# Kernel optimization log

Measured on AMD Instinct MI355X. Metric: run time of the kernel, lower is better.

The kernel has to match this reference:

```python
import jax, jax.numpy as jnp
import numpy as np

B, T, C = 4, 2048, 1024
NH = 16
HD = C // NH  # 64

def setup_inputs() -> dict:
    key = jax.random.key(0)
    k1, k2, k3 = jax.random.split(key, 3)
    x = jax.random.normal(k1, (B, T, C), dtype=jnp.float32)
    w_qkv = jax.random.normal(k2, (C, 3 * C), dtype=jnp.float32) * (1.0 / np.sqrt(C))
    w_out = jax.random.normal(k3, (C, C), dtype=jnp.float32) * (1.0 / np.sqrt(C))
    b_out = jnp.zeros((C,), dtype=jnp.float32)
    return {"x": x, "w_qkv": w_qkv, "w_out": w_out, "b_out": b_out}

def reference(x, w_qkv, w_out, b_out):
    b, t, c = x.shape
    nh, hd = NH, c // NH
    qkv = x @ w_qkv                      # [b, t, 3c]
    q, k, v = jnp.split(qkv, 3, axis=-1)
    # [b, t, c] -> [b, nh, t, hd]
    def heads(z):
        return z.reshape(b, t, nh, hd).transpose(0, 2, 1, 3)
    q, k, v = heads(q), heads(k), heads(v)
    scale = 1.0 / jnp.sqrt(jnp.asarray(hd, dtype=x.dtype))
    scores = jnp.einsum('bhqd,bhkd->bhqk', q, k) * scale  # [b, nh, t, t]
    causal = jnp.tril(jnp.ones((t, t), dtype=bool))
    scores = jnp.where(causal, scores, jnp.asarray(-jnp.inf, dtype=scores.dtype))
    attn = jax.nn.softmax(scores, axis=-1)
    ctx = jnp.einsum('bhqk,bhkd->bhqd', attn, v)           # [b, nh, t, hd]
    ctx = ctx.transpose(0, 2, 1, 3).reshape(b, t, c)
    return ctx @ w_out + b_out
```

## Files before the change

kernel.cpp:

```cpp
#include <hip/hip_runtime.h>
#include <cmath>


typedef __bf16 bf16x4 __attribute__((ext_vector_type(4)));
typedef __bf16 bf16x8 __attribute__((ext_vector_type(8)));
typedef float  f32x4  __attribute__((ext_vector_type(4)));
typedef float  f32x16 __attribute__((ext_vector_type(16)));

__device__ __forceinline__ void gload_lds16(const __bf16* g, __bf16* l) {
    __builtin_amdgcn_global_load_lds(
        (const __attribute__((address_space(1))) void*)g,
        (__attribute__((address_space(3))) void*)l,
        16, 0, 0);
}

__global__ __launch_bounds__(256) void cast_bf16(const float* __restrict__ in,
                                                 __bf16* __restrict__ out, int n4) {
    int i = blockIdx.x * 256 + threadIdx.x;
    if (i >= n4) return;
    float4 f = *(const float4*)(in + (size_t)i * 4);
    bf16x4 o;
    o[0] = (__bf16)f.x; o[1] = (__bf16)f.y; o[2] = (__bf16)f.z; o[3] = (__bf16)f.w;
    *(bf16x4*)(out + (size_t)i * 4) = o;
}

__global__ __launch_bounds__(256) void transpose_cast(const float* __restrict__ W,
                                                      __bf16* __restrict__ WT,
                                                      int K, int N) {
    __shared__ float tile[32][33];
    const int n0 = blockIdx.x * 32, k0 = blockIdx.y * 32;
    const int tx = threadIdx.x & 31, ty = threadIdx.x >> 5;
    #pragma unroll
    for (int i = 0; i < 4; ++i)
        tile[ty + 8 * i][tx] = W[(size_t)(k0 + ty + 8 * i) * N + n0 + tx];
    __syncthreads();
    #pragma unroll
    for (int i = 0; i < 4; ++i)
        WT[(size_t)(n0 + ty + 8 * i) * K + k0 + tx] = (__bf16)tile[tx][ty + 8 * i];
}

__global__ __launch_bounds__(256) void transpose_v(const __bf16* __restrict__ qkv,
                                                   __bf16* __restrict__ Vt) {
    constexpr int T = 2048, R3C = 3072;
    __shared__ __bf16 tile[64][72];
    const int bh = blockIdx.y;
    const int b  = bh >> 4, h = bh & 15;
    const int kt = blockIdx.x * 64;
    const int tid = threadIdx.x;
    #pragma unroll
    for (int i = 0; i < 2; ++i) {
        int idx = tid + 256 * i;
        int kr  = idx >> 3;
        int c8  = idx & 7;
        *(uint4*)&tile[kr][c8 * 8] =
            *(const uint4*)(qkv + (size_t)(b * T + kt + kr) * R3C + 2048 + h * 64 + c8 * 8);
    }
    __syncthreads();
    #pragma unroll
    for (int i = 0; i < 2; ++i) {
        int idx = tid + 256 * i;
        int d   = idx >> 3;
        int k8  = idx & 7;
        union { __bf16 v[8]; uint4 u; } t;
        #pragma unroll
        for (int j = 0; j < 8; ++j) t.v[j] = tile[k8 * 8 + j][d];
        *(uint4*)(Vt + ((size_t)bh * 64 + d) * T + kt + k8 * 8) = t.u;
    }
}

template <typename OutT, bool BIAS>
__global__ __launch_bounds__(256) void gemm_bt(const __bf16* __restrict__ A,
                                               const __bf16* __restrict__ BT,
                                               OutT* __restrict__ Cc,
                                               const float* __restrict__ bias,
                                               int M, int N, int K) {
    __shared__ __bf16 As[128 * 32];
    __shared__ __bf16 Bs[128 * 32];

    const int tid  = threadIdx.x;
    const int lane = tid & 63;
    const int w    = tid >> 6;
    const int wr   = w >> 1, wc = w & 1;
    const int cc   = lane & 15, gg = lane >> 4;
    const int rowBase = blockIdx.y * 128;
    const int colBase = blockIdx.x * 128;

    f32x4 acc[4][4];
    #pragma unroll
    for (int i = 0; i < 4; ++i)
        #pragma unroll
        for (int j = 0; j < 4; ++j) acc[i][j] = f32x4{0.f, 0.f, 0.f, 0.f};

    for (int k0 = 0; k0 < K; k0 += 32) {
        __syncthreads();
        #pragma unroll
        for (int i = 0; i < 2; ++i) {
            int idx = tid + 256 * i;
            int r   = idx >> 2;
            int c4  = idx & 3;
            gload_lds16(A  + (size_t)(rowBase + r) * K + k0 + c4 * 8, &As[idx * 8]);
            gload_lds16(BT + (size_t)(colBase + r) * K + k0 + c4 * 8, &Bs[idx * 8]);
        }
        __syncthreads();

        bf16x8 af[4], bfr[4];
        #pragma unroll
        for (int i = 0; i < 4; ++i)
            af[i] = *(const bf16x8*)&As[(wr * 64 + i * 16 + cc) * 32 + gg * 8];
        #pragma unroll
        for (int j = 0; j < 4; ++j)
            bfr[j] = *(const bf16x8*)&Bs[(wc * 64 + j * 16 + cc) * 32 + gg * 8];
        #pragma unroll
        for (int i = 0; i < 4; ++i)
            #pragma unroll
            for (int j = 0; j < 4; ++j)
                acc[i][j] = __builtin_amdgcn_mfma_f32_16x16x32_bf16(af[i], bfr[j], acc[i][j], 0, 0, 0);
    }

    #pragma unroll
    for (int i = 0; i < 4; ++i)
        #pragma unroll
        for (int j = 0; j < 4; ++j) {
            const int col = colBase + wc * 64 + j * 16 + cc;
            #pragma unroll
            for (int r = 0; r < 4; ++r) {
                const int row = rowBase + wr * 64 + i * 16 + gg * 4 + r;
                float v = acc[i][j][r];
                if (BIAS) v += bias[col];
                Cc[(size_t)row * N + col] = (OutT)v;
            }
        }
}

__global__ __launch_bounds__(256) void flash_attn_mfma(const __bf16* __restrict__ qkv,
                                                       const __bf16* __restrict__ Vt,
                                                       __bf16* __restrict__ ctx) {
    constexpr int T = 2048, C = 1024, NH = 16, HD = 64;
    constexpr int R3C = 3 * C;
    constexpr float K1 = 0.125f * 1.44269504088896f;
    constexpr float K2 = -16.0f * 1.44269504088896f;

    const int tid  = threadIdx.x;
    const int lane = tid & 63;
    const int w    = tid >> 6;
    const int q5   = lane & 31;
    const int half = lane >> 5;

    const int bh   = blockIdx.x;
    const int y    = blockIdx.y;
    const int qtA  = 15 - y;
    const int qtB  = y;
    const int b    = bh >> 4;
    const int h    = bh & 15;
    const int srowA = qtA * 128 + w * 32;
    const int srowB = qtB * 128 + w * 32;
    const int ktmaxA = qtA * 128 + 64;
    const int ktmaxB = qtB * 128 + 64;

    __shared__ __attribute__((aligned(16))) __bf16 Ks [64][72];
    __shared__ __attribute__((aligned(16))) __bf16 VsT[64][72];
    __shared__ __attribute__((aligned(16))) __bf16 Ps [4][32][72];

    const __bf16* QrowA = qkv + (size_t)(b * T + srowA + q5) * R3C + h * HD;
    const __bf16* QrowB = qkv + (size_t)(b * T + srowB + q5) * R3C + h * HD;
    bf16x8 QbA[4], QbB[4];
    #pragma unroll
    for (int ks = 0; ks < 4; ++ks) {
        QbA[ks] = *(const bf16x8*)(QrowA + ks * 16 + half * 8);
        QbB[ks] = *(const bf16x8*)(QrowB + ks * 16 + half * 8);
    }

    f32x16 OA[2], OB[2];
    #pragma unroll
    for (int mb = 0; mb < 2; ++mb)
        #pragma unroll
        for (int r = 0; r < 16; ++r) { OA[mb][r] = 0.f; OB[mb][r] = 0.f; }
    float lsumA = 0.f, lsumB = 0.f;

    const __bf16* Kb  = qkv + (size_t)(b * T) * R3C + C + h * HD;
    const __bf16* Vtb = Vt + (size_t)bh * 64 * T;

    for (int kt = 0; kt <= ktmaxA; kt += 64) {
        __syncthreads();
        #pragma unroll
        for (int i = 0; i < 2; ++i) {
            int idx = tid + 256 * i;
            int kr  = idx >> 3;
            int c8  = idx & 7;
            *(uint4*)&Ks[kr][c8 * 8] = *(const uint4*)(Kb + (size_t)(kt + kr) * R3C + c8 * 8);
        }
        #pragma unroll
        for (int i = 0; i < 2; ++i) {
            int idx = tid + 256 * i;
            int d   = idx >> 3;
            int k8  = idx & 7;
            *(uint4*)&VsT[d][k8 * 8] = *(const uint4*)(Vtb + (size_t)d * T + kt + k8 * 8);
        }
        __syncthreads();

        #pragma unroll
        for (int sub = 0; sub < 2; ++sub) {
            f32x16 S;
            #pragma unroll
            for (int r = 0; r < 16; ++r) S[r] = 0.f;
            #pragma unroll
            for (int ks = 0; ks < 4; ++ks) {
                bf16x8 kb = *(const bf16x8*)&Ks[sub * 32 + q5][ks * 16 + half * 8];
                S = __builtin_amdgcn_mfma_f32_32x32x16_bf16(kb, QbA[ks], S, 0, 0, 0);
            }
            if (kt + sub * 32 + 31 > srowA) {
                #pragma unroll
                for (int r = 0; r < 16; ++r) {
                    int key = kt + sub * 32 + (r & 3) + 8 * (r >> 2) + 4 * half;
                    if (key > srowA + q5) S[r] = -1e30f;
                }
            }
            #pragma unroll
            for (int a = 0; a < 4; ++a) {
                union { bf16x4 v; uint2 u; } pk;
                #pragma unroll
                for (int bq = 0; bq < 4; ++bq) {
                    float p = exp2f(fmaf(S[4 * a + bq], K1, K2));
                    lsumA += p;
                    pk.v[bq] = (__bf16)p;
                }
                *(uint2*)&Ps[w][q5][sub * 32 + 8 * a + 4 * half] = pk.u;
            }
        }
        #pragma unroll
        for (int ks2 = 0; ks2 < 4; ++ks2) {
            bf16x8 pa = *(const bf16x8*)&Ps[w][q5][ks2 * 16 + half * 8];
            #pragma unroll
            for (int mb = 0; mb < 2; ++mb) {
                bf16x8 vb = *(const bf16x8*)&VsT[mb * 32 + q5][ks2 * 16 + half * 8];
                OA[mb] = __builtin_amdgcn_mfma_f32_32x32x16_bf16(vb, pa, OA[mb], 0, 0, 0);
            }
        }

        if (kt <= ktmaxB) {
            #pragma unroll
            for (int sub = 0; sub < 2; ++sub) {
                f32x16 S;
                #pragma unroll
                for (int r = 0; r < 16; ++r) S[r] = 0.f;
                #pragma unroll
                for (int ks = 0; ks < 4; ++ks) {
                    bf16x8 kb = *(const bf16x8*)&Ks[sub * 32 + q5][ks * 16 + half * 8];
                    S = __builtin_amdgcn_mfma_f32_32x32x16_bf16(kb, QbB[ks], S, 0, 0, 0);
                }
                if (kt + sub * 32 + 31 > srowB) {
                    #pragma unroll
                    for (int r = 0; r < 16; ++r) {
                        int key = kt + sub * 32 + (r & 3) + 8 * (r >> 2) + 4 * half;
                        if (key > srowB + q5) S[r] = -1e30f;
                    }
                }
                #pragma unroll
                for (int a = 0; a < 4; ++a) {
                    union { bf16x4 v; uint2 u; } pk;
                    #pragma unroll
                    for (int bq = 0; bq < 4; ++bq) {
                        float p = exp2f(fmaf(S[4 * a + bq], K1, K2));
                        lsumB += p;
                        pk.v[bq] = (__bf16)p;
                    }
                    *(uint2*)&Ps[w][q5][sub * 32 + 8 * a + 4 * half] = pk.u;
                }
            }
            #pragma unroll
            for (int ks2 = 0; ks2 < 4; ++ks2) {
                bf16x8 pa = *(const bf16x8*)&Ps[w][q5][ks2 * 16 + half * 8];
                #pragma unroll
                for (int mb = 0; mb < 2; ++mb) {
                    bf16x8 vb = *(const bf16x8*)&VsT[mb * 32 + q5][ks2 * 16 + half * 8];
                    OB[mb] = __builtin_amdgcn_mfma_f32_32x32x16_bf16(vb, pa, OB[mb], 0, 0, 0);
                }
            }
        }
    }

    const float invA = 1.f / (lsumA + __shfl_xor(lsumA, 32));
    const float invB = 1.f / (lsumB + __shfl_xor(lsumB, 32));

    __bf16* crowA = ctx + (size_t)(b * T + srowA + q5) * C + h * HD;
    __bf16* crowB = ctx + (size_t)(b * T + srowB + q5) * C + h * HD;
    #pragma unroll
    for (int mb = 0; mb < 2; ++mb)
        #pragma unroll
        for (int a = 0; a < 4; ++a) {
            union { bf16x4 v; uint2 u; } pA, pB;
            #pragma unroll
            for (int bq = 0; bq < 4; ++bq) {
                pA.v[bq] = (__bf16)(OA[mb][4 * a + bq] * invA);
                pB.v[bq] = (__bf16)(OB[mb][4 * a + bq] * invB);
            }
            *(uint2*)(crowA + mb * 32 + 8 * a + 4 * half) = pA.u;
            *(uint2*)(crowB + mb * 32 + 8 * a + 4 * half) = pB.u;
        }
}

extern "C" void kernel_launch(void* const* d_in, const int* in_sizes, int n_in,
                              void* d_out, int out_size, void* d_ws, size_t ws_size,
                              hipStream_t stream) {
    constexpr int B = 4, T = 2048, C = 1024;
    constexpr int M = B * T;

    const float* x     = (const float*)d_in[0];
    const float* w_qkv = (const float*)d_in[1];
    const float* w_out = (const float*)d_in[2];
    const float* b_out = (const float*)d_in[3];
    float* out = (float*)d_out;

    char* ws = (char*)d_ws;
    __bf16* xb     = (__bf16*)(ws);
    __bf16* wqkvT  = (__bf16*)(ws + (16ull << 20));
    __bf16* woutT  = (__bf16*)(ws + (22ull << 20));
    __bf16* qkvb   = (__bf16*)(ws + (24ull << 20));
    __bf16* ctxb   = (__bf16*)(ws + (72ull << 20));
    __bf16* Vt     = (__bf16*)(ws + (88ull << 20));

    cast_bf16<<<(M * C / 4 + 255) / 256, 256, 0, stream>>>(x, xb, M * C / 4);
    transpose_cast<<<dim3(3 * C / 32, C / 32), 256, 0, stream>>>(w_qkv, wqkvT, C, 3 * C);
    transpose_cast<<<dim3(C / 32, C / 32), 256, 0, stream>>>(w_out, woutT, C, C);

    gemm_bt<__bf16, false><<<dim3(3 * C / 128, M / 128), 256, 0, stream>>>(
        xb, wqkvT, qkvb, nullptr, M, 3 * C, C);

    transpose_v<<<dim3(T / 64, B * 16), 256, 0, stream>>>(qkvb, Vt);

    flash_attn_mfma<<<dim3(B * 16, 8), 256, 0, stream>>>(qkvb, Vt, ctxb);

    gemm_bt<float, true><<<dim3(C / 128, M / 128), 256, 0, stream>>>(
        ctxb, woutT, out, b_out, M, C, C);
}
```

Baseline: 286.5 us.

## Add pipelined 256x256 QKV GEMM and keep attention P in registers

```diff
diff --git a/kernel.cpp b/kernel.cpp
--- a/kernel.cpp
+++ b/kernel.cpp
@@ -13,6 +13,20 @@
         (__attribute__((address_space(3))) void*)l,
         16, 0, 0);
 }
+
+__device__ __forceinline__ unsigned packbf(float a, float b) {
+    union { __bf16 h[2]; unsigned u; } t;
+    t.h[0] = (__bf16)a; t.h[1] = (__bf16)b;
+    return t.u;
+}
+
+__device__ __forceinline__ void permswap(unsigned& a, unsigned& b) {
+    asm volatile("v_permlane32_swap_b32 %0, %1" : "+v"(a), "+v"(b));
+}
+
+#define BAR()  __builtin_amdgcn_s_barrier()
+#define VM2()  { asm volatile("s_waitcnt vmcnt(2)" ::: "memory"); \
+                 __builtin_amdgcn_sched_barrier(0); }
 
 __global__ __launch_bounds__(256) void cast_bf16(const float* __restrict__ in,
                                                  __bf16* __restrict__ out, int n4) {
@@ -68,6 +82,121 @@
     }
 }
 
+__global__ __launch_bounds__(512) void gemm256(const __bf16* __restrict__ A,
+                                               const __bf16* __restrict__ BT,
+                                               __bf16* __restrict__ Cc,
+                                               int M, int N, int K) {
+    __shared__ __attribute__((aligned(16))) char lds[131072];
+    const int tid = threadIdx.x, lane = tid & 63, w = tid >> 6;
+    const int wr = w >> 2, wc = w & 3, cc = lane & 15, gg = lane >> 4;
+
+    const int cpx = gridDim.x >> 3;
+    const int swz = ((int)blockIdx.x & 7) * cpx + ((int)blockIdx.x >> 3);
+    const int nbx = N >> 8;
+    const int rowBase = (swz / nbx) << 8;
+    const int colBase = (swz % nbx) << 8;
+    const int NT = K >> 6;
+
+    const int sChunk = (lane & 7) ^ (lane >> 3);
+    const int rsub   = lane >> 3;
+
+    auto stA = [&](int t, int h) {
+        const int buf = t & 1, k0 = (t % NT) * 64;
+        #pragma unroll
+        for (int l = 0; l < 2; ++l) {
+            int idx   = l * 8 + w;
+            int rbase = ((idx >> 3) << 7) + h * 64 + ((idx & 7) << 3);
+            gload_lds16(A + (size_t)(rowBase + rbase + rsub) * K + k0 + sChunk * 8,
+                        (__bf16*)(lds + buf * 65536 + rbase * 128 + lane * 16));
+        }
+    };
+    auto stB = [&](int t, int h) {
+        const int buf = t & 1, k0 = (t % NT) * 64;
+        #pragma unroll
+        for (int l = 0; l < 2; ++l) {
+            int idx   = l * 8 + w;
+            int rbase = ((idx >> 2) << 6) + h * 32 + ((idx & 3) << 3);
+            gload_lds16(BT + (size_t)(colBase + rbase + rsub) * K + k0 + sChunk * 8,
+                        (__bf16*)(lds + buf * 65536 + 32768 + rbase * 128 + lane * 16));
+        }
+    };
+
+    f32x4 acc[8][4];
+    #pragma unroll
+    for (int i = 0; i < 8; ++i)
+        #pragma unroll
+        for (int j = 0; j < 4; ++j) acc[i][j] = f32x4{0.f, 0.f, 0.f, 0.f};
+    bf16x8 afr[8], bfr[8];
+
+    auto rdA = [&](int buf, int mh) {
+        const char* base = lds + buf * 65536;
+        #pragma unroll
+        for (int i = 0; i < 4; ++i)
+            #pragma unroll
+            for (int kk = 0; kk < 2; ++kk) {
+                int r  = wr * 128 + mh * 64 + i * 16 + cc;
+                int cb = (kk * 64 + gg * 16) ^ ((cc & 7) << 4);
+                afr[i * 2 + kk] = *(const bf16x8*)(base + r * 128 + cb);
+            }
+    };
+    auto rdB = [&](int buf) {
+        const char* base = lds + buf * 65536 + 32768;
+        #pragma unroll
+        for (int j = 0; j < 4; ++j)
+            #pragma unroll
+            for (int kk = 0; kk < 2; ++kk) {
+                int r  = wc * 64 + j * 16 + cc;
+                int cb = (kk * 64 + gg * 16) ^ ((cc & 7) << 4);
+                bfr[j * 2 + kk] = *(const bf16x8*)(base + r * 128 + cb);
+            }
+    };
+
+#define QMFMA(MH, NH)                                                        \
+    _Pragma("unroll") for (int i = 0; i < 4; ++i)                            \
+    _Pragma("unroll") for (int j = 0; j < 2; ++j)                            \
+    _Pragma("unroll") for (int kk = 0; kk < 2; ++kk)                         \
+        acc[(MH)*4 + i][(NH)*2 + j] = __builtin_amdgcn_mfma_f32_16x16x32_bf16( \
+            afr[i*2 + kk], bfr[((NH)*2 + j)*2 + kk], acc[(MH)*4 + i][(NH)*2 + j], 0, 0, 0);
+
+    stA(0, 0); stB(0, 0); stA(0, 1); stB(0, 1); stA(1, 0);
+    VM2(); BAR();
+
+    for (int t = 0; t < NT; ++t) {
+        const int buf = t & 1;
+        rdA(buf, 0); rdB(buf);
+        stB(t + 1, 0);
+        BAR();
+        __builtin_amdgcn_s_setprio(1); QMFMA(0, 0); __builtin_amdgcn_s_setprio(0);
+        BAR();
+        stA(t + 1, 1);
+        BAR();
+        __builtin_amdgcn_s_setprio(1); QMFMA(0, 1); __builtin_amdgcn_s_setprio(0);
+        BAR();
+        rdA(buf, 1);
+        stB(t + 1, 1);
+        BAR();
+        __builtin_amdgcn_s_setprio(1); QMFMA(1, 0); __builtin_amdgcn_s_setprio(0);
+        BAR();
+        stA(t + 2, 0);
+        BAR();
+        __builtin_amdgcn_s_setprio(1); QMFMA(1, 1); __builtin_amdgcn_s_setprio(0);
+        VM2(); BAR();
+    }
+#undef QMFMA
+
+    #pragma unroll
+    for (int i = 0; i < 8; ++i)
+        #pragma unroll
+        for (int j = 0; j < 4; ++j) {
+            const int col = colBase + wc * 64 + j * 16 + cc;
+            #pragma unroll
+            for (int rr = 0; rr < 4; ++rr) {
+                const int row = rowBase + wr * 128 + (i >> 2) * 64 + (i & 3) * 16 + gg * 4 + rr;
+                Cc[(size_t)row * N + col] = (__bf16)acc[i][j][rr];
+            }
+        }
+}
+
 template <typename OutT, bool BIAS>
 __global__ __launch_bounds__(256) void gemm_bt(const __bf16* __restrict__ A,
                                                const __bf16* __restrict__ BT,
@@ -103,18 +232,18 @@
         }
         __syncthreads();
 
-        bf16x8 af[4], bfr[4];
+        bf16x8 af[4], bfr2[4];
         #pragma unroll
         for (int i = 0; i < 4; ++i)
             af[i] = *(const bf16x8*)&As[(wr * 64 + i * 16 + cc) * 32 + gg * 8];
         #pragma unroll
         for (int j = 0; j < 4; ++j)
-            bfr[j] = *(const bf16x8*)&Bs[(wc * 64 + j * 16 + cc) * 32 + gg * 8];
+            bfr2[j] = *(const bf16x8*)&Bs[(wc * 64 + j * 16 + cc) * 32 + gg * 8];
         #pragma unroll
         for (int i = 0; i < 4; ++i)
             #pragma unroll
             for (int j = 0; j < 4; ++j)
-                acc[i][j] = __builtin_amdgcn_mfma_f32_16x16x32_bf16(af[i], bfr[j], acc[i][j], 0, 0, 0);
+                acc[i][j] = __builtin_amdgcn_mfma_f32_16x16x32_bf16(af[i], bfr2[j], acc[i][j], 0, 0, 0);
     }
 
     #pragma unroll
@@ -135,7 +264,7 @@
 __global__ __launch_bounds__(256) void flash_attn_mfma(const __bf16* __restrict__ qkv,
                                                        const __bf16* __restrict__ Vt,
                                                        __bf16* __restrict__ ctx) {
-    constexpr int T = 2048, C = 1024, NH = 16, HD = 64;
+    constexpr int T = 2048, C = 1024, HD = 64;
     constexpr int R3C = 3 * C;
     constexpr float K1 = 0.125f * 1.44269504088896f;
     constexpr float K2 = -16.0f * 1.44269504088896f;
@@ -159,7 +288,6 @@
 
     __shared__ __attribute__((aligned(16))) __bf16 Ks [64][72];
     __shared__ __attribute__((aligned(16))) __bf16 VsT[64][72];
-    __shared__ __attribute__((aligned(16))) __bf16 Ps [4][32][72];
 
     const __bf16* QrowA = qkv + (size_t)(b * T + srowA + q5) * R3C + h * HD;
     const __bf16* QrowB = qkv + (size_t)(b * T + srowB + q5) * R3C + h * HD;
@@ -198,84 +326,60 @@
         }
         __syncthreads();
 
-        #pragma unroll
-        for (int sub = 0; sub < 2; ++sub) {
+        auto subtile = [&](int sub, const bf16x8* Qb, int srow, f32x16* O, float& lsum) {
             f32x16 S;
             #pragma unroll
             for (int r = 0; r < 16; ++r) S[r] = 0.f;
             #pragma unroll
             for (int ks = 0; ks < 4; ++ks) {
                 bf16x8 kb = *(const bf16x8*)&Ks[sub * 32 + q5][ks * 16 + half * 8];
-                S = __builtin_amdgcn_mfma_f32_32x32x16_bf16(kb, QbA[ks], S, 0, 0, 0);
-            }
-            if (kt + sub * 32 + 31 > srowA) {
+                S = __builtin_amdgcn_mfma_f32_32x32x16_bf16(kb, Qb[ks], S, 0, 0, 0);
+            }
+            if (kt + sub * 32 + 31 > srow) {
                 #pragma unroll
                 for (int r = 0; r < 16; ++r) {
                     int key = kt + sub * 32 + (r & 3) + 8 * (r >> 2) + 4 * half;
-                    if (key > srowA + q5) S[r] = -1e30f;
+                    if (key > srow + q5) S[r] = -1e30f;
                 }
             }
-            #pragma unroll
-            for (int a = 0; a < 4; ++a) {
-                union { bf16x4 v; uint2 u; } pk;
-                #pragma unroll
-                for (int bq = 0; bq < 4; ++bq) {
-                    float p = exp2f(fmaf(S[4 * a + bq], K1, K2));
-                    lsumA += p;
-                    pk.v[bq] = (__bf16)p;
-                }
-                *(uint2*)&Ps[w][q5][sub * 32 + 8 * a + 4 * half] = pk.u;
-            }
-        }
-        #pragma unroll
-        for (int ks2 = 0; ks2 < 4; ++ks2) {
-            bf16x8 pa = *(const bf16x8*)&Ps[w][q5][ks2 * 16 + half * 8];
+            float p[16];
+            #pragma unroll
+            for (int r = 0; r < 16; ++r) {
+                p[r] = exp2f(fmaf(S[r], K1, K2));
+                lsum += p[r];
+            }
+            unsigned w0 = packbf(p[0],  p[1]);
+            unsigned w1 = packbf(p[2],  p[3]);
+            unsigned w2 = packbf(p[4],  p[5]);
+            unsigned w3 = packbf(p[6],  p[7]);
+            permswap(w0, w2);
+            permswap(w1, w3);
+            unsigned w4 = packbf(p[8],  p[9]);
+            unsigned w5 = packbf(p[10], p[11]);
+            unsigned w6 = packbf(p[12], p[13]);
+            unsigned w7 = packbf(p[14], p[15]);
+            permswap(w4, w6);
+            permswap(w5, w7);
+            union { unsigned u[4]; bf16x8 v; } pf0, pf1;
+            pf0.u[0] = w0; pf0.u[1] = w1; pf0.u[2] = w2; pf0.u[3] = w3;
+            pf1.u[0] = w4; pf1.u[1] = w5; pf1.u[2] = w6; pf1.u[3] = w7;
+            const int vc = sub * 32 + half * 8;
             #pragma unroll
             for (int mb = 0; mb < 2; ++mb) {
-                bf16x8 vb = *(const bf16x8*)&VsT[mb * 32 + q5][ks2 * 16 + half * 8];
-                OA[mb] = __builtin_amdgcn_mfma_f32_32x32x16_bf16(vb, pa, OA[mb], 0, 0, 0);
-            }
-        }
-
+                bf16x8 v0 = *(const bf16x8*)&VsT[mb * 32 + q5][vc];
+                O[mb] = __builtin_amdgcn_mfma_f32_32x32x16_bf16(v0, pf0.v, O[mb], 0, 0, 0);
+                bf16x8 v1 = *(const bf16x8*)&VsT[mb * 32 + q5][vc + 16];
+                O[mb] = __builtin_amdgcn_mfma_f32_32x32x16_bf16(v1, pf1.v, O[mb], 0, 0, 0);
+            }
+        };
+
+        #pragma unroll
+        for (int sub = 0; sub < 2; ++sub)
+            subtile(sub, QbA, srowA, OA, lsumA);
         if (kt <= ktmaxB) {
             #pragma unroll
-            for (int sub = 0; sub < 2; ++sub) {
-                f32x16 S;
-                #pragma unroll
-                for (int r = 0; r < 16; ++r) S[r] = 0.f;
-                #pragma unroll
-                for (int ks = 0; ks < 4; ++ks) {
-                    bf16x8 kb = *(const bf16x8*)&Ks[sub * 32 + q5][ks * 16 + half * 8];
-                    S = __builtin_amdgcn_mfma_f32_32x32x16_bf16(kb, QbB[ks], S, 0, 0, 0);
-                }
-                if (kt + sub * 32 + 31 > srowB) {
-                    #pragma unroll
-                    for (int r = 0; r < 16; ++r) {
-                        int key = kt + sub * 32 + (r & 3) + 8 * (r >> 2) + 4 * half;
-                        if (key > srowB + q5) S[r] = -1e30f;
-                    }
-                }
-                #pragma unroll
-                for (int a = 0; a < 4; ++a) {
-                    union { bf16x4 v; uint2 u; } pk;
-                    #pragma unroll
-                    for (int bq = 0; bq < 4; ++bq) {
-                        float p = exp2f(fmaf(S[4 * a + bq], K1, K2));
-                        lsumB += p;
-                        pk.v[bq] = (__bf16)p;
-                    }
-                    *(uint2*)&Ps[w][q5][sub * 32 + 8 * a + 4 * half] = pk.u;
-                }
-            }
-            #pragma unroll
-            for (int ks2 = 0; ks2 < 4; ++ks2) {
-                bf16x8 pa = *(const bf16x8*)&Ps[w][q5][ks2 * 16 + half * 8];
-                #pragma unroll
-                for (int mb = 0; mb < 2; ++mb) {
-                    bf16x8 vb = *(const bf16x8*)&VsT[mb * 32 + q5][ks2 * 16 + half * 8];
-                    OB[mb] = __builtin_amdgcn_mfma_f32_32x32x16_bf16(vb, pa, OB[mb], 0, 0, 0);
-                }
-            }
+            for (int sub = 0; sub < 2; ++sub)
+                subtile(sub, QbB, srowB, OB, lsumB);
         }
     }
 
@@ -323,8 +427,7 @@
     transpose_cast<<<dim3(3 * C / 32, C / 32), 256, 0, stream>>>(w_qkv, wqkvT, C, 3 * C);
     transpose_cast<<<dim3(C / 32, C / 32), 256, 0, stream>>>(w_out, woutT, C, C);
 
-    gemm_bt<__bf16, false><<<dim3(3 * C / 128, M / 128), 256, 0, stream>>>(
-        xb, wqkvT, qkvb, nullptr, M, 3 * C, C);
+    gemm256<<<384, 512, 0, stream>>>(xb, wqkvT, qkvb, M, 3 * C, C);
 
     transpose_v<<<dim3(T / 64, B * 16), 256, 0, stream>>>(qkvb, Vt);
 
```

After: 280.8 us. -2.0%, faster.
